# Kernel tuning notes

Measured on AMD Instinct MI355X. Metric: run time of the kernel, lower is better.

The kernel has to match this reference:

```python
import jax, jax.numpy as jnp
import numpy as np

IN, H, B = 256, 256, 65536


def setup_inputs() -> dict:
    key = jax.random.key(0)
    ks = jax.random.split(key, 20)
    s_in = 1.0 / np.sqrt(IN)
    s_h = 1.0 / np.sqrt(H)
    d = {
        "input": jax.random.normal(ks[0], (B, IN), jnp.float32),
        "hidden": jax.random.normal(ks[1], (B, H), jnp.float32),
        "cell": jax.random.normal(ks[2], (B, H), jnp.float32),
    }
    names_i = ["Wif", "Wii", "Wio", "Wig"]
    names_h = ["Whf", "Whi", "Who", "Whg"]
    for j, n in enumerate(names_i):
        d[n] = jax.random.uniform(ks[3 + j], (H, IN), jnp.float32, -s_in, s_in)
        d["b" + n[1:]] = jax.random.uniform(ks[7 + j], (H,), jnp.float32, -s_in, s_in)
    for j, n in enumerate(names_h):
        d[n] = jax.random.uniform(ks[11 + j], (H, H), jnp.float32, -s_h, s_h)
        d["b" + n[1:]] = jax.random.uniform(ks[15 + j], (H,), jnp.float32, -s_h, s_h)
    return d


def reference(input, hidden, cell,
              Wif, bif, Wii, bii, Wio, bio, Wig, big,
              Whf, bhf, Whi, bhi, Who, bho, Whg, bhg):
    # Fuse the 8 small linears into two [*,4H] GEMMs (same math as 8 separate Linear calls)
    Wi = jnp.concatenate([Wif, Wii, Wio, Wig], axis=0)  # [4H, IN]
    Wh = jnp.concatenate([Whf, Whi, Who, Whg], axis=0)  # [4H, H]
    bi = jnp.concatenate([bif, bii, bio, big])
    bh = jnp.concatenate([bhf, bhi, bho, bhg])
    gates = input @ Wi.T + bi + hidden @ Wh.T + bh  # [B, 4H]
    f, i, o, g = jnp.split(gates, 4, axis=1)
    f = jax.nn.sigmoid(f)
    i = jax.nn.sigmoid(i)
    o = jax.nn.sigmoid(o)
    g = jnp.tanh(g)
    new_cell = f * cell + i * g
    new_hidden = o * jnp.tanh(new_cell)
    output = jax.nn.log_softmax(new_hidden, axis=1)
    return output, new_hidden, new_cell
```

## Files before the change

kernel.cpp:

```cpp
#include <hip/hip_runtime.h>
#include <hip/hip_bf16.h>
#include <stdint.h>


#define BH 16777216

typedef float f32x4 __attribute__((ext_vector_type(4)));
typedef short short8 __attribute__((ext_vector_type(8)));

__device__ __forceinline__ unsigned short f2bf(float f) {
    union { float f; unsigned u; } v; v.f = f;
    unsigned u = v.u;
    return (unsigned short)((u + 0x7fffu + ((u >> 16) & 1u)) >> 16);
}

__device__ __forceinline__ unsigned pack2bf(float a, float b) {
    __hip_bfloat162 h = __float22bfloat162_rn(make_float2(a, b));
    union { __hip_bfloat162 h; unsigned u; } v; v.h = h;
    return v.u;
}

__device__ __forceinline__ float sigm(float x) { return 1.f / (1.f + __expf(-x)); }
__device__ __forceinline__ float tanh_(float x) { return 1.f - 2.f / (1.f + __expf(2.f * x)); }

__device__ __forceinline__ void glds16(const void* g, const void* l) {
    __builtin_amdgcn_global_load_lds(
        (const __attribute__((address_space(1))) unsigned int*)(uintptr_t)g,
        (__attribute__((address_space(3))) unsigned int*)(unsigned int)(uintptr_t)l,
        16, 0, 0);
}

__global__ __launch_bounds__(256) void pack_kernel(
    const float* __restrict__ Wif, const float* __restrict__ Wii,
    const float* __restrict__ Wio, const float* __restrict__ Wig,
    const float* __restrict__ Whf, const float* __restrict__ Whi,
    const float* __restrict__ Who, const float* __restrict__ Whg,
    const float* __restrict__ bif, const float* __restrict__ bii,
    const float* __restrict__ bio, const float* __restrict__ big,
    const float* __restrict__ bhf, const float* __restrict__ bhi,
    const float* __restrict__ bho, const float* __restrict__ bhg,
    unsigned short* __restrict__ wpack, float* __restrict__ bpack)
{
    const int t = blockIdx.x * 256 + threadIdx.x;
    const int n16  = t & 15;
    const int kg   = (t >> 4) & 3;
    const int Nt   = (t >> 6) & 15;
    const int step = (t >> 10) & 15;
    const int hg   = t >> 14;
    const int gate = Nt & 3;
    const int wc   = Nt >> 2;
    const int h    = hg * 64 + wc * 16 + n16;
    const int k0   = step * 32 + kg * 8;

    const float* Wi = (gate == 0) ? Wif : (gate == 1) ? Wii : (gate == 2) ? Wio : Wig;
    const float* Wh = (gate == 0) ? Whf : (gate == 1) ? Whi : (gate == 2) ? Who : Whg;
    const float* src = (k0 < 256) ? (Wi + h * 256 + k0) : (Wh + h * 256 + (k0 - 256));

    unsigned pk[4];
#pragma unroll
    for (int p = 0; p < 4; ++p)
        pk[p] = (unsigned)f2bf(src[p * 2]) | ((unsigned)f2bf(src[p * 2 + 1]) << 16);
    uint4 o4 = {pk[0], pk[1], pk[2], pk[3]};
    *(uint4*)&wpack[(size_t)t * 8] = o4;

    if (t < 1024) {
        const int cp = t;
        const int n2 = cp & 15, Nt2 = (cp >> 4) & 15, hg2 = cp >> 8;
        const int g2 = Nt2 & 3, wc2 = Nt2 >> 2;
        const int h2 = hg2 * 64 + wc2 * 16 + n2;
        const float* bi = (g2 == 0) ? bif : (g2 == 1) ? bii : (g2 == 2) ? bio : big;
        const float* bh = (g2 == 0) ? bhf : (g2 == 1) ? bhi : (g2 == 2) ? bho : bhg;
        bpack[cp] = bi[h2] + bh[h2];
    }
}

__global__ __launch_bounds__(256) void convert_kernel(
    const float* __restrict__ input, const float* __restrict__ hidden,
    unsigned short* __restrict__ xpack)
{
    const int t = blockIdx.x * 256 + threadIdx.x;
    const int l     = t & 63;
    const int rt    = (t >> 6) & 7;
    const int step  = (t >> 9) & 15;
    const int panel = t >> 13;
    const int row = panel * 128 + rt * 16 + (l & 15);
    const int k0  = step * 32 + (l >> 4) * 8;
    const float* src = (k0 < 256) ? input + (size_t)row * 256 + k0
                                  : hidden + (size_t)row * 256 + (k0 - 256);
    float4 x0 = *(const float4*)src;
    float4 x1 = *(const float4*)(src + 4);
    uint4 o; o.x = pack2bf(x0.x, x0.y); o.y = pack2bf(x0.z, x0.w);
    o.z = pack2bf(x1.x, x1.y); o.w = pack2bf(x1.z, x1.w);
    *(uint4*)&xpack[(size_t)t * 8] = o;
}

__global__ __launch_bounds__(512, 4) void lstm_gemm_kernel(
    const unsigned short* __restrict__ xpack,
    const float* __restrict__ cell,
    const unsigned short* __restrict__ wpack, const float* __restrict__ bpack,
    float* __restrict__ out)
{
    __shared__ unsigned short buf[3][12288];

    const int swz = (blockIdx.x & 7) * 256 + (blockIdx.x >> 3);
    const int hg    = swz & 3;
    const int panel = swz >> 2;
    const int row0  = panel * 128;

    const int tid = threadIdx.x;
    const int w = tid >> 6, l = tid & 63;
    const int wr = w >> 2, wc = w & 3;

    const unsigned short* asrc = xpack + (size_t)panel * 65536 + w * 512 + l * 8;
    const unsigned short* wsrc = wpack + (size_t)hg * 131072 + w * 1024 + l * 8;

#define STAGE(s)                                                              \
    do {                                                                      \
        glds16(asrc + (size_t)(s) * 4096, &buf[(s) % 3][w * 512]);            \
        glds16(wsrc + (size_t)(s) * 8192, &buf[(s) % 3][4096 + w * 1024]);    \
        glds16(wsrc + (size_t)(s) * 8192 + 512,                               \
               &buf[(s) % 3][4096 + w * 1024 + 512]);                         \
    } while (0)

    STAGE(0);
    STAGE(1);

    f32x4 acc[4][4] = {};

#pragma unroll
    for (int k = 0; k < 16; ++k) {
        const int cur = k % 3;
        if (k < 14) asm volatile("s_waitcnt vmcnt(3)" ::: "memory");
        else        asm volatile("s_waitcnt vmcnt(0)" ::: "memory");
        __builtin_amdgcn_s_barrier();

        short8 Af[4], Bf[4];
#pragma unroll
        for (int m = 0; m < 4; ++m)
            Af[m] = *(const short8*)&buf[cur][((wr * 4 + m) * 64 + l) << 3];
#pragma unroll
        for (int n = 0; n < 4; ++n)
            Bf[n] = *(const short8*)&buf[cur][4096 + (((wc * 4 + n) * 64 + l) << 3)];

        if (k + 2 < 16) STAGE(k + 2);

        __builtin_amdgcn_s_setprio(1);
#pragma unroll
        for (int m = 0; m < 4; ++m)
#pragma unroll
            for (int n = 0; n < 4; ++n)
                acc[m][n] = __builtin_amdgcn_mfma_f32_16x16x32_bf16(Af[m], Bf[n], acc[m][n], 0, 0, 0);
        __builtin_amdgcn_s_setprio(0);
    }
#undef STAGE

    const int n16l = l & 15;
    const int lrow = l >> 4;
    const int hcol = hg * 64 + wc * 16 + n16l;
    float bias[4];
#pragma unroll
    for (int n = 0; n < 4; ++n)
        bias[n] = bpack[hg * 256 + wc * 64 + n * 16 + n16l];

#pragma unroll
    for (int m = 0; m < 4; ++m) {
#pragma unroll
        for (int rr = 0; rr < 4; ++rr) {
            const size_t rg_ = (size_t)row0 + wr * 64 + m * 16 + lrow * 4 + rr;
            const float fv = sigm(acc[m][0][rr] + bias[0]);
            const float iv = sigm(acc[m][1][rr] + bias[1]);
            const float ov = sigm(acc[m][2][rr] + bias[2]);
            const float gv = tanh_(acc[m][3][rr] + bias[3]);
            const float cv = cell[rg_ * 256 + hcol];
            const float nc = fv * cv + iv * gv;
            const float nhv = ov * tanh_(nc);
            out[(size_t)2 * BH + rg_ * 256 + hcol] = nc;
            out[(size_t)BH + rg_ * 256 + hcol] = nhv;
        }
    }
}

__global__ __launch_bounds__(256) void softmax_kernel(
    const float* __restrict__ nh, float* __restrict__ outp)
{
    const int w = threadIdx.x >> 6, l = threadIdx.x & 63;
#pragma unroll 1
    for (int it = 0; it < 8; ++it) {
        const size_t row = (size_t)it * 8192 + blockIdx.x * 4 + w;
        float4 v = *(const float4*)(nh + row * 256 + l * 4);
        float s = __expf(v.x) + __expf(v.y) + __expf(v.z) + __expf(v.w);
#pragma unroll
        for (int m = 1; m < 64; m <<= 1) s += __shfl_xor(s, m);
        const float lz = __logf(s);
        float4 o = {v.x - lz, v.y - lz, v.z - lz, v.w - lz};
        *(float4*)(outp + row * 256 + l * 4) = o;
    }
}

extern "C" void kernel_launch(void* const* d_in, const int* in_sizes, int n_in,
                              void* d_out, int out_size, void* d_ws, size_t ws_size,
                              hipStream_t stream)
{
    const float* input  = (const float*)d_in[0];
    const float* hidden = (const float*)d_in[1];
    const float* cell   = (const float*)d_in[2];
    const float* Wif = (const float*)d_in[3];  const float* bif = (const float*)d_in[4];
    const float* Wii = (const float*)d_in[5];  const float* bii = (const float*)d_in[6];
    const float* Wio = (const float*)d_in[7];  const float* bio = (const float*)d_in[8];
    const float* Wig = (const float*)d_in[9];  const float* big = (const float*)d_in[10];
    const float* Whf = (const float*)d_in[11]; const float* bhf = (const float*)d_in[12];
    const float* Whi = (const float*)d_in[13]; const float* bhi = (const float*)d_in[14];
    const float* Who = (const float*)d_in[15]; const float* bho = (const float*)d_in[16];
    const float* Whg = (const float*)d_in[17]; const float* bhg = (const float*)d_in[18];

    unsigned short* wpack = (unsigned short*)d_ws;
    float* bpack = (float*)((char*)d_ws + (size_t)1024 * 512 * 2);

    float* out = (float*)d_out;
    unsigned short* xpack = (unsigned short*)d_out;

    hipLaunchKernelGGL(pack_kernel, dim3(256), dim3(256), 0, stream,
        Wif, Wii, Wio, Wig, Whf, Whi, Who, Whg,
        bif, bii, bio, big, bhf, bhi, bho, bhg, wpack, bpack);

    hipLaunchKernelGGL(convert_kernel, dim3(16384), dim3(256), 0, stream,
        input, hidden, xpack);

    hipLaunchKernelGGL(lstm_gemm_kernel, dim3(2048), dim3(512), 0, stream,
        xpack, cell, wpack, bpack, out);

    hipLaunchKernelGGL(softmax_kernel, dim3(2048), dim3(256), 0, stream,
        out + (size_t)BH, out);
}
```

Before: 171.9 us.

## Shrink GEMM tile to 128x128 with 4 waves and double buffering

The LSTM GEMM block tile shrinks from 128 rows by 256 gate-columns (8 waves, triple-buffered LDS) to 128 by 128 (4 waves, double-buffered LDS), and the grid doubles to 4096 blocks. The weight pack layout is reorganised to match the 32-hidden-unit column groups. The aim is to cut LDS per block and raise occupancy and block count. The cost is that each A panel is loaded twice as often, and the pipeline now waits with vmcnt(0) every step, so prefetch is only one stage ahead.

Result: no change. 174.4 us (+1.4%).

```diff
diff --git a/kernel.cpp b/kernel.cpp
--- a/kernel.cpp
+++ b/kernel.cpp
@@ -42,15 +42,14 @@
     unsigned short* __restrict__ wpack, float* __restrict__ bpack)
 {
     const int t = blockIdx.x * 256 + threadIdx.x;
-    const int n16  = t & 15;
-    const int kg   = (t >> 4) & 3;
-    const int Nt   = (t >> 6) & 15;
-    const int step = (t >> 10) & 15;
-    const int hg   = t >> 14;
-    const int gate = Nt & 3;
-    const int wc   = Nt >> 2;
-    const int h    = hg * 64 + wc * 16 + n16;
-    const int k0   = step * 32 + kg * 8;
+    const int l    = t & 63;
+    const int Nt8  = (t >> 6) & 7;
+    const int step = (t >> 9) & 15;
+    const int cg   = t >> 13;
+    const int gate = Nt8 & 3;
+    const int wn2  = Nt8 >> 2;
+    const int h    = cg * 32 + wn2 * 16 + (l & 15);
+    const int k0   = step * 32 + (l >> 4) * 8;
 
     const float* Wi = (gate == 0) ? Wif : (gate == 1) ? Wii : (gate == 2) ? Wio : Wig;
     const float* Wh = (gate == 0) ? Whf : (gate == 1) ? Whi : (gate == 2) ? Who : Whg;
@@ -65,9 +64,8 @@
 
     if (t < 1024) {
         const int cp = t;
-        const int n2 = cp & 15, Nt2 = (cp >> 4) & 15, hg2 = cp >> 8;
-        const int g2 = Nt2 & 3, wc2 = Nt2 >> 2;
-        const int h2 = hg2 * 64 + wc2 * 16 + n2;
+        const int n2 = cp & 15, g2 = (cp >> 4) & 3, w2 = (cp >> 6) & 1, cg2 = cp >> 7;
+        const int h2 = cg2 * 32 + w2 * 16 + n2;
         const float* bi = (g2 == 0) ? bif : (g2 == 1) ? bii : (g2 == 2) ? bio : big;
         const float* bh = (g2 == 0) ? bhf : (g2 == 1) ? bhi : (g2 == 2) ? bho : bhg;
         bpack[cp] = bi[h2] + bh[h2];
@@ -94,55 +92,54 @@
     *(uint4*)&xpack[(size_t)t * 8] = o;
 }
 
-__global__ __launch_bounds__(512, 4) void lstm_gemm_kernel(
+__global__ __launch_bounds__(256, 4) void lstm_gemm_kernel(
     const unsigned short* __restrict__ xpack,
     const float* __restrict__ cell,
     const unsigned short* __restrict__ wpack, const float* __restrict__ bpack,
     float* __restrict__ out)
 {
-    __shared__ unsigned short buf[3][12288];
-
-    const int swz = (blockIdx.x & 7) * 256 + (blockIdx.x >> 3);
-    const int hg    = swz & 3;
-    const int panel = swz >> 2;
+    __shared__ unsigned short buf[2][8192];
+
+    const int swz = (blockIdx.x & 7) * 512 + (blockIdx.x >> 3);
+    const int cg    = swz & 7;
+    const int panel = swz >> 3;
     const int row0  = panel * 128;
 
     const int tid = threadIdx.x;
     const int w = tid >> 6, l = tid & 63;
-    const int wr = w >> 2, wc = w & 3;
-
-    const unsigned short* asrc = xpack + (size_t)panel * 65536 + w * 512 + l * 8;
-    const unsigned short* wsrc = wpack + (size_t)hg * 131072 + w * 1024 + l * 8;
-
-#define STAGE(s)                                                              \
+    const int wm = w >> 1, wn2 = w & 1;
+    const int n16 = l & 15;
+
+    const unsigned short* asrc = xpack + (size_t)panel * 65536 + l * 8;
+    const unsigned short* wsrc = wpack + (size_t)cg * 65536 + l * 8;
+
+#define STAGE(s, bb)                                                          \
     do {                                                                      \
-        glds16(asrc + (size_t)(s) * 4096, &buf[(s) % 3][w * 512]);            \
-        glds16(wsrc + (size_t)(s) * 8192, &buf[(s) % 3][4096 + w * 1024]);    \
-        glds16(wsrc + (size_t)(s) * 8192 + 512,                               \
-               &buf[(s) % 3][4096 + w * 1024 + 512]);                         \
+        glds16(asrc + (size_t)(s) * 4096 + (w)     * 512, &buf[bb][(w)     * 512]); \
+        glds16(asrc + (size_t)(s) * 4096 + (w + 4) * 512, &buf[bb][(w + 4) * 512]); \
+        glds16(wsrc + (size_t)(s) * 4096 + (w)     * 512, &buf[bb][4096 + (w)     * 512]); \
+        glds16(wsrc + (size_t)(s) * 4096 + (w + 4) * 512, &buf[bb][4096 + (w + 4) * 512]); \
     } while (0)
 
-    STAGE(0);
-    STAGE(1);
+    STAGE(0, 0);
 
     f32x4 acc[4][4] = {};
 
 #pragma unroll
     for (int k = 0; k < 16; ++k) {
-        const int cur = k % 3;
-        if (k < 14) asm volatile("s_waitcnt vmcnt(3)" ::: "memory");
-        else        asm volatile("s_waitcnt vmcnt(0)" ::: "memory");
+        const int cb = k & 1, nb = cb ^ 1;
+        asm volatile("s_waitcnt vmcnt(0)" ::: "memory");
         __builtin_amdgcn_s_barrier();
 
         short8 Af[4], Bf[4];
 #pragma unroll
         for (int m = 0; m < 4; ++m)
-            Af[m] = *(const short8*)&buf[cur][((wr * 4 + m) * 64 + l) << 3];
+            Af[m] = *(const short8*)&buf[cb][((wm * 4 + m) * 64 + l) << 3];
 #pragma unroll
         for (int n = 0; n < 4; ++n)
-            Bf[n] = *(const short8*)&buf[cur][4096 + (((wc * 4 + n) * 64 + l) << 3)];
-
-        if (k + 2 < 16) STAGE(k + 2);
+            Bf[n] = *(const short8*)&buf[cb][4096 + (((wn2 * 4 + n) * 64 + l) << 3)];
+
+        if (k < 15) STAGE(k + 1, nb);
 
         __builtin_amdgcn_s_setprio(1);
 #pragma unroll
@@ -154,19 +151,18 @@
     }
 #undef STAGE
 
-    const int n16l = l & 15;
     const int lrow = l >> 4;
-    const int hcol = hg * 64 + wc * 16 + n16l;
+    const int hcol = cg * 32 + wn2 * 16 + n16;
     float bias[4];
 #pragma unroll
     for (int n = 0; n < 4; ++n)
-        bias[n] = bpack[hg * 256 + wc * 64 + n * 16 + n16l];
+        bias[n] = bpack[cg * 128 + wn2 * 64 + n * 16 + n16];
 
 #pragma unroll
     for (int m = 0; m < 4; ++m) {
 #pragma unroll
         for (int rr = 0; rr < 4; ++rr) {
-            const size_t rg_ = (size_t)row0 + wr * 64 + m * 16 + lrow * 4 + rr;
+            const size_t rg_ = (size_t)row0 + wm * 64 + m * 16 + lrow * 4 + rr;
             const float fv = sigm(acc[m][0][rr] + bias[0]);
             const float iv = sigm(acc[m][1][rr] + bias[1]);
             const float ov = sigm(acc[m][2][rr] + bias[2]);
@@ -226,7 +222,7 @@
     hipLaunchKernelGGL(convert_kernel, dim3(16384), dim3(256), 0, stream,
         input, hidden, xpack);
 
-    hipLaunchKernelGGL(lstm_gemm_kernel, dim3(2048), dim3(512), 0, stream,
+    hipLaunchKernelGGL(lstm_gemm_kernel, dim3(4096), dim3(256), 0, stream,
         xpack, cell, wpack, bpack, out);
 
     hipLaunchKernelGGL(softmax_kernel, dim3(2048), dim3(256), 0, stream,
```
